# Kernel optimization log

Measured on AMD Instinct MI355X. Metric: run time of the kernel, lower is better.

## Reference

```python
import jax, jax.numpy as jnp
import numpy as np

BATCH = 4096
DIM = 128
TEMP = 0.5
EPS = 1e-8


def _neg_mask(batch):
    n = 2 * batch
    m = np.ones((n, n), dtype=bool)
    np.fill_diagonal(m, False)
    idx = np.arange(batch)
    m[idx, idx + batch] = False
    m[idx + batch, idx] = False
    return m


def setup_inputs() -> dict:
    key = jax.random.key(0)
    k1, k2 = jax.random.split(key)
    zx = jax.random.normal(k1, (BATCH, DIM), dtype=jnp.float32)
    zy = jax.random.normal(k2, (BATCH, DIM), dtype=jnp.float32)
    return {"zx": zx, "zy": zy}


def reference(zx, zy):
    batch = zx.shape[0]
    n = 2 * batch  # N = 2 * batch_size
    z = jnp.concatenate([zx, zy], axis=0)  # [N, D]
    # cosine similarity = normalized GEMM (avoids O(N^2*D) intermediate)
    norm = jnp.maximum(jnp.linalg.norm(z, axis=1, keepdims=True), EPS)
    zn = z / norm
    sim = (zn @ zn.T) / TEMP  # [N, N]
    # positives: diagonals at offsets +batch and -batch
    sim_xy = jnp.diagonal(sim, offset=batch)
    sim_yx = jnp.diagonal(sim, offset=-batch)
    positives = jnp.concatenate([sim_xy, sim_yx]).reshape(n, 1)  # [N, 1]
    # negatives: mask out diagonal and positive pairs (static boolean mask)
    mask = _neg_mask(batch)
    negatives = sim[mask].reshape(n, n - 2)  # [N, N-2]
    logits = jnp.concatenate([positives, negatives], axis=1)  # [N, N-1]
    # CrossEntropy(labels=0, reduction='sum') / N
    loss = jnp.sum(jax.nn.logsumexp(logits, axis=1) - logits[:, 0]) / n
    return loss
```

## Files before the change

kernel.cpp:

```cpp
#include <hip/hip_runtime.h>
#include <hip/hip_bf16.h>

#define BATCH 4096
#define NROWS 8192
#define DIM   128

typedef __bf16 bf16x8 __attribute__((ext_vector_type(8)));
typedef __bf16 bf16x2 __attribute__((ext_vector_type(2)));
typedef float  f32x4  __attribute__((ext_vector_type(4)));


__global__ __launch_bounds__(256) void normalize_kernel(
    const float* __restrict__ zx, const float* __restrict__ zy,
    ushort* __restrict__ zn, float* __restrict__ S)
{
  const int tid  = threadIdx.x;
  const int lane = tid & 63;
  const int w    = tid >> 6;
  const int row  = blockIdx.x * 4 + w;
  const float* src = (row < BATCH) ? (zx + (size_t)row * DIM)
                                   : (zy + (size_t)(row - BATCH) * DIM);
  float2 v = ((const float2*)src)[lane];
  float ss = v.x * v.x + v.y * v.y;
#pragma unroll
  for (int off = 1; off < 64; off <<= 1)
    ss += __shfl_xor(ss, off, 64);
  float inv = 1.0f / fmaxf(sqrtf(ss), 1e-8f);
  bf16x2 st;
  st.x = (__bf16)(v.x * inv);
  st.y = (__bf16)(v.y * inv);
  ushort* dst = zn + (size_t)(row >> 7) * 16384 + (row & 127) * 8;
  *reinterpret_cast<bf16x2*>(dst + (lane >> 2) * 1024 + (lane & 3) * 2) = st;
  if (lane == 0) S[row] = 0.f;
}

__global__ __launch_bounds__(256, 3) void simloss_kernel(
    const ushort* __restrict__ zn, float* __restrict__ S, float* __restrict__ P)
{
  const int tid  = threadIdx.x;
  const int lane = tid & 63;
  const int w    = tid >> 6;
  const int wr   = w >> 1, wc = w & 1;
  const int q    = lane >> 4;
  const int l15  = lane & 15;

  const int t = blockIdx.x;
  int rb = (int)(0.5f * (129.0f - sqrtf((float)(16641 - 8 * t))));
  while (rb * (129 - rb) / 2 > t) --rb;
  while ((rb + 1) * (128 - rb) / 2 <= t) ++rb;
  const int cb = rb + (t - rb * (129 - rb) / 2);

  const int R0 = rb * 128, C0 = cb * 128;
  const bool diag = (rb == cb);
  const bool part = (cb == rb + 32);

  const ushort* At = zn + (size_t)rb * 16384;
  const ushort* Bt = zn + (size_t)cb * 16384;

  f32x4 acc[4][4];
#pragma unroll
  for (int mi = 0; mi < 4; ++mi)
#pragma unroll
    for (int ni = 0; ni < 4; ++ni)
      acc[mi][ni] = (f32x4){0.f, 0.f, 0.f, 0.f};

#pragma unroll
  for (int ks = 0; ks < 4; ++ks) {
    const int ck = (ks * 4 + q) * 1024;
    bf16x8 af[4], bf[4];
#pragma unroll
    for (int mi = 0; mi < 4; ++mi)
      af[mi] = *reinterpret_cast<const bf16x8*>(At + ck + (wr * 64 + mi * 16 + l15) * 8);
#pragma unroll
    for (int ni = 0; ni < 4; ++ni)
      bf[ni] = *reinterpret_cast<const bf16x8*>(Bt + ck + (wc * 64 + ni * 16 + l15) * 8);
#pragma unroll
    for (int mi = 0; mi < 4; ++mi)
#pragma unroll
      for (int ni = 0; ni < 4; ++ni)
        acc[mi][ni] = __builtin_amdgcn_mfma_f32_16x16x32_bf16(
            af[mi], bf[ni], acc[mi][ni], 0, 0, 0);
  }

  const float K1 = 2.8853900817779268f;

  float Srow[4][4];
  float Scol[4] = {0.f, 0.f, 0.f, 0.f};
#pragma unroll
  for (int mi = 0; mi < 4; ++mi)
#pragma unroll
    for (int r = 0; r < 4; ++r) Srow[mi][r] = 0.f;

#pragma unroll
  for (int mi = 0; mi < 4; ++mi)
#pragma unroll
    for (int ni = 0; ni < 4; ++ni)
#pragma unroll
      for (int r = 0; r < 4; ++r) {
        const float v = __builtin_amdgcn_exp2f(fmaf(acc[mi][ni][r], K1, -K1));
        Srow[mi][r] += v;
        Scol[ni] += v;
      }

  if (diag) {
    if (wr == wc) {
#pragma unroll
      for (int mi = 0; mi < 4; ++mi)
#pragma unroll
        for (int r = 0; r < 4; ++r) {
          const float v = __builtin_amdgcn_exp2f(fmaf(acc[mi][mi][r], K1, -K1));
          if (l15 == q * 4 + r) Srow[mi][r] -= v;
        }
    }
  } else {
#pragma unroll
    for (int ni = 0; ni < 4; ++ni) {
      float v = Scol[ni];
      v += __shfl_xor(v, 16, 64);
      v += __shfl_xor(v, 32, 64);
      if (q == 0)
        atomicAdd(&S[C0 + wc * 64 + ni * 16 + l15], v);
    }
  }

#pragma unroll
  for (int mi = 0; mi < 4; ++mi)
#pragma unroll
    for (int r = 0; r < 4; ++r) {
      float v = Srow[mi][r];
      v += __shfl_xor(v, 1, 64);
      v += __shfl_xor(v, 2, 64);
      v += __shfl_xor(v, 4, 64);
      v += __shfl_xor(v, 8, 64);
      if (l15 == 0)
        atomicAdd(&S[R0 + wr * 64 + mi * 16 + q * 4 + r], v);
    }

  if (part) {
#pragma unroll
    for (int mi = 0; mi < 4; ++mi)
#pragma unroll
      for (int ni = 0; ni < 4; ++ni)
#pragma unroll
        for (int r = 0; r < 4; ++r) {
          const int rl = wr * 64 + mi * 16 + q * 4 + r;
          const int cl = wc * 64 + ni * 16 + l15;
          if (rl == cl) {
            const float p = 2.0f * acc[mi][ni][r];
            P[R0 + rl] = p;
            P[C0 + cl] = p;
          }
        }
  }
}

__global__ __launch_bounds__(1024) void finalize_kernel(
    const float* __restrict__ S, const float* __restrict__ P,
    float* __restrict__ out)
{
  float c = 0.f;
  for (int i = threadIdx.x; i < NROWS; i += 1024)
    c += 2.0f + __logf(S[i]) - P[i];
#pragma unroll
  for (int off = 1; off < 64; off <<= 1)
    c += __shfl_xor(c, off, 64);
  __shared__ float wsum[16];
  const int lane = threadIdx.x & 63, w = threadIdx.x >> 6;
  if (lane == 0) wsum[w] = c;
  __syncthreads();
  if (threadIdx.x == 0) {
    float s = 0.f;
#pragma unroll
    for (int k = 0; k < 16; ++k) s += wsum[k];
    out[0] = s * (1.0f / NROWS);
  }
}

extern "C" void kernel_launch(void* const* d_in, const int* in_sizes, int n_in,
                              void* d_out, int out_size, void* d_ws, size_t ws_size,
                              hipStream_t stream)
{
  const float* zx = (const float*)d_in[0];
  const float* zy = (const float*)d_in[1];
  ushort* zn = (ushort*)d_ws;
  float*  S  = (float*)((char*)d_ws + (size_t)NROWS * DIM * 2);
  float*  P  = S + NROWS;
  float*  out = (float*)d_out;

  normalize_kernel<<<NROWS / 4, 256, 0, stream>>>(zx, zy, zn, S);
  simloss_kernel<<<2080, 256, 0, stream>>>(zn, S, P);
  finalize_kernel<<<1, 1024, 0, stream>>>(S, P, out);
}
```

Before: 99.57 us.

## Process four tiles per block with LDS double-buffered B and register-resident A

Each block now walks four consecutive upper-triangle tiles instead of one. It keeps the A row-block fragments in registers across tiles that share a row and flushes row sums only when the row changes. B tiles are staged into a double-buffered LDS array with global_load_lds so the next tile's load overlaps the current MFMA and exp work. Atomics switch to unsafeAtomicAdd. The grid shrinks to 520 blocks with launch bounds of 2 waves per EU, which trades parallelism and occupancy for fewer redundant A loads and fewer row atomics.

```diff
diff --git a/kernel.cpp b/kernel.cpp
--- a/kernel.cpp
+++ b/kernel.cpp
@@ -8,6 +8,11 @@
 typedef __bf16 bf16x8 __attribute__((ext_vector_type(8)));
 typedef __bf16 bf16x2 __attribute__((ext_vector_type(2)));
 typedef float  f32x4  __attribute__((ext_vector_type(4)));
+
+typedef const __attribute__((address_space(1))) unsigned int* gptr_t;
+typedef __attribute__((address_space(3))) unsigned int* lptr_t;
+
+__device__ inline void atomAdd(float* p, float v) { unsafeAtomicAdd(p, v); }
 
 
 __global__ __launch_bounds__(256) void normalize_kernel(
@@ -34,124 +39,165 @@
   if (lane == 0) S[row] = 0.f;
 }
 
-__global__ __launch_bounds__(256, 3) void simloss_kernel(
+__global__ __launch_bounds__(256, 2) void simloss_kernel(
     const ushort* __restrict__ zn, float* __restrict__ S, float* __restrict__ P)
 {
+  __shared__ ushort Ls[2][16384];
+
   const int tid  = threadIdx.x;
   const int lane = tid & 63;
   const int w    = tid >> 6;
   const int wr   = w >> 1, wc = w & 1;
   const int q    = lane >> 4;
   const int l15  = lane & 15;
-
-  const int t = blockIdx.x;
-  int rb = (int)(0.5f * (129.0f - sqrtf((float)(16641 - 8 * t))));
-  while (rb * (129 - rb) / 2 > t) --rb;
-  while ((rb + 1) * (128 - rb) / 2 <= t) ++rb;
-  const int cb = rb + (t - rb * (129 - rb) / 2);
-
-  const int R0 = rb * 128, C0 = cb * 128;
-  const bool diag = (rb == cb);
-  const bool part = (cb == rb + 32);
-
-  const ushort* At = zn + (size_t)rb * 16384;
-  const ushort* Bt = zn + (size_t)cb * 16384;
-
-  f32x4 acc[4][4];
+  const float K1 = 2.8853900817779268f;
+
+  const int t0 = blockIdx.x * 4;
+  int rb = (int)(0.5f * (129.0f - sqrtf((float)(16641 - 8 * t0))));
+  while (rb * (129 - rb) / 2 > t0) --rb;
+  while ((rb + 1) * (128 - rb) / 2 <= t0) ++rb;
+  int cb = rb + (t0 - rb * (129 - rb) / 2);
+
+  int rbs[4], cbs[4];
+#pragma unroll
+  for (int i = 0; i < 4; ++i) {
+    rbs[i] = rb; cbs[i] = cb;
+    if (++cb > 63) { ++rb; cb = rb; }
+  }
+
+  auto stageB = [&](int tb, int buf) {
+    const ushort* src = zn + (size_t)tb * 16384;
+#pragma unroll
+    for (int j = 0; j < 8; ++j) {
+      const int off = (j * 256 + w * 64) * 8;
+      __builtin_amdgcn_global_load_lds((gptr_t)(src + off + lane * 8),
+                                       (lptr_t)(&Ls[buf][off]), 16, 0, 0);
+    }
+  };
+
+  bf16x8 af[4][4];
+  auto loadA = [&](int arb) {
+#pragma unroll
+    for (int ks = 0; ks < 4; ++ks) {
+      const ushort* ap = zn + (size_t)arb * 16384 + (ks * 4 + q) * 1024
+                       + (wr * 64 + l15) * 8;
+#pragma unroll
+      for (int mi = 0; mi < 4; ++mi)
+        af[mi][ks] = *reinterpret_cast<const bf16x8*>(ap + mi * 16 * 8);
+    }
+  };
+
+  float Srow[4][4];
 #pragma unroll
   for (int mi = 0; mi < 4; ++mi)
 #pragma unroll
-    for (int ni = 0; ni < 4; ++ni)
-      acc[mi][ni] = (f32x4){0.f, 0.f, 0.f, 0.f};
-
-#pragma unroll
-  for (int ks = 0; ks < 4; ++ks) {
-    const int ck = (ks * 4 + q) * 1024;
-    bf16x8 af[4], bf[4];
+    for (int r = 0; r < 4; ++r) Srow[mi][r] = 0.f;
+
+  auto flushRows = [&](int arb) {
 #pragma unroll
     for (int mi = 0; mi < 4; ++mi)
-      af[mi] = *reinterpret_cast<const bf16x8*>(At + ck + (wr * 64 + mi * 16 + l15) * 8);
-#pragma unroll
-    for (int ni = 0; ni < 4; ++ni)
-      bf[ni] = *reinterpret_cast<const bf16x8*>(Bt + ck + (wc * 64 + ni * 16 + l15) * 8);
+#pragma unroll
+      for (int r = 0; r < 4; ++r) {
+        float v = Srow[mi][r];
+        v += __shfl_xor(v, 1, 64);
+        v += __shfl_xor(v, 2, 64);
+        v += __shfl_xor(v, 4, 64);
+        v += __shfl_xor(v, 8, 64);
+        if (l15 == 0)
+          atomAdd(&S[arb * 128 + wr * 64 + mi * 16 + q * 4 + r], v);
+        Srow[mi][r] = 0.f;
+      }
+  };
+
+  stageB(cbs[0], 0);
+  loadA(rbs[0]);
+  int curA = rbs[0];
+  __syncthreads();
+
+  for (int i = 0; i < 4; ++i) {
+    if (i < 3) stageB(cbs[i + 1], (i + 1) & 1);
+    if (rbs[i] != curA) { flushRows(curA); loadA(rbs[i]); curA = rbs[i]; }
+
+    const ushort* Bp = Ls[i & 1];
+    const int C0 = cbs[i] * 128, R0 = rbs[i] * 128;
+    const bool diag = (cbs[i] == rbs[i]);
+    const bool part = (cbs[i] == rbs[i] + 32);
+
+    f32x4 acc[4][4];
 #pragma unroll
     for (int mi = 0; mi < 4; ++mi)
 #pragma unroll
       for (int ni = 0; ni < 4; ++ni)
-        acc[mi][ni] = __builtin_amdgcn_mfma_f32_16x16x32_bf16(
-            af[mi], bf[ni], acc[mi][ni], 0, 0, 0);
+        acc[mi][ni] = (f32x4){0.f, 0.f, 0.f, 0.f};
+
+#pragma unroll
+    for (int ks = 0; ks < 4; ++ks) {
+      const int ck = (ks * 4 + q) * 1024;
+      bf16x8 bf[4];
+#pragma unroll
+      for (int ni = 0; ni < 4; ++ni)
+        bf[ni] = *reinterpret_cast<const bf16x8*>(Bp + ck + (wc * 64 + ni * 16 + l15) * 8);
+#pragma unroll
+      for (int mi = 0; mi < 4; ++mi)
+#pragma unroll
+        for (int ni = 0; ni < 4; ++ni)
+          acc[mi][ni] = __builtin_amdgcn_mfma_f32_16x16x32_bf16(
+              af[mi][ks], bf[ni], acc[mi][ni], 0, 0, 0);
+    }
+
+    float Scol[4] = {0.f, 0.f, 0.f, 0.f};
+#pragma unroll
+    for (int mi = 0; mi < 4; ++mi)
+#pragma unroll
+      for (int ni = 0; ni < 4; ++ni)
+#pragma unroll
+        for (int r = 0; r < 4; ++r) {
+          const float v = __builtin_amdgcn_exp2f(fmaf(acc[mi][ni][r], K1, -K1));
+          Srow[mi][r] += v;
+          Scol[ni] += v;
+        }
+
+    if (diag) {
+      if (wr == wc) {
+#pragma unroll
+        for (int mi = 0; mi < 4; ++mi)
+#pragma unroll
+          for (int r = 0; r < 4; ++r) {
+            const float v = __builtin_amdgcn_exp2f(fmaf(acc[mi][mi][r], K1, -K1));
+            if (l15 == q * 4 + r) Srow[mi][r] -= v;
+          }
+      }
+    } else {
+#pragma unroll
+      for (int ni = 0; ni < 4; ++ni) {
+        float v = Scol[ni];
+        v += __shfl_xor(v, 16, 64);
+        v += __shfl_xor(v, 32, 64);
+        if (q == 0)
+          atomAdd(&S[C0 + wc * 64 + ni * 16 + l15], v);
+      }
+    }
+
+    if (part) {
+#pragma unroll
+      for (int mi = 0; mi < 4; ++mi)
+#pragma unroll
+        for (int ni = 0; ni < 4; ++ni)
+#pragma unroll
+          for (int r = 0; r < 4; ++r) {
+            const int rl = wr * 64 + mi * 16 + q * 4 + r;
+            const int cl = wc * 64 + ni * 16 + l15;
+            if (rl == cl) {
+              const float p = 2.0f * acc[mi][ni][r];
+              P[R0 + rl] = p;
+              P[C0 + cl] = p;
+            }
+          }
+    }
+
+    __syncthreads();
   }
-
-  const float K1 = 2.8853900817779268f;
-
-  float Srow[4][4];
-  float Scol[4] = {0.f, 0.f, 0.f, 0.f};
-#pragma unroll
-  for (int mi = 0; mi < 4; ++mi)
-#pragma unroll
-    for (int r = 0; r < 4; ++r) Srow[mi][r] = 0.f;
-
-#pragma unroll
-  for (int mi = 0; mi < 4; ++mi)
-#pragma unroll
-    for (int ni = 0; ni < 4; ++ni)
-#pragma unroll
-      for (int r = 0; r < 4; ++r) {
-        const float v = __builtin_amdgcn_exp2f(fmaf(acc[mi][ni][r], K1, -K1));
-        Srow[mi][r] += v;
-        Scol[ni] += v;
-      }
-
-  if (diag) {
-    if (wr == wc) {
-#pragma unroll
-      for (int mi = 0; mi < 4; ++mi)
-#pragma unroll
-        for (int r = 0; r < 4; ++r) {
-          const float v = __builtin_amdgcn_exp2f(fmaf(acc[mi][mi][r], K1, -K1));
-          if (l15 == q * 4 + r) Srow[mi][r] -= v;
-        }
-    }
-  } else {
-#pragma unroll
-    for (int ni = 0; ni < 4; ++ni) {
-      float v = Scol[ni];
-      v += __shfl_xor(v, 16, 64);
-      v += __shfl_xor(v, 32, 64);
-      if (q == 0)
-        atomicAdd(&S[C0 + wc * 64 + ni * 16 + l15], v);
-    }
-  }
-
-#pragma unroll
-  for (int mi = 0; mi < 4; ++mi)
-#pragma unroll
-    for (int r = 0; r < 4; ++r) {
-      float v = Srow[mi][r];
-      v += __shfl_xor(v, 1, 64);
-      v += __shfl_xor(v, 2, 64);
-      v += __shfl_xor(v, 4, 64);
-      v += __shfl_xor(v, 8, 64);
-      if (l15 == 0)
-        atomicAdd(&S[R0 + wr * 64 + mi * 16 + q * 4 + r], v);
-    }
-
-  if (part) {
-#pragma unroll
-    for (int mi = 0; mi < 4; ++mi)
-#pragma unroll
-      for (int ni = 0; ni < 4; ++ni)
-#pragma unroll
-        for (int r = 0; r < 4; ++r) {
-          const int rl = wr * 64 + mi * 16 + q * 4 + r;
-          const int cl = wc * 64 + ni * 16 + l15;
-          if (rl == cl) {
-            const float p = 2.0f * acc[mi][ni][r];
-            P[R0 + rl] = p;
-            P[C0 + cl] = p;
-          }
-        }
-  }
+  flushRows(curA);
 }
 
 __global__ __launch_bounds__(1024) void finalize_kernel(
@@ -188,6 +234,6 @@
   float*  out = (float*)d_out;
 
   normalize_kernel<<<NROWS / 4, 256, 0, stream>>>(zx, zy, zn, S);
-  simloss_kernel<<<2080, 256, 0, stream>>>(zn, S, P);
+  simloss_kernel<<<520, 256, 0, stream>>>(zn, S, P);
   finalize_kernel<<<1, 1024, 0, stream>>>(S, P, out);
 }
```

Measured after the change: 95.50 us. 4.1% less time.
